# Kernel tuning notes

Hardware: AMD Instinct MI355X
Metric: run time of the kernel (lower is better)

## Reference

```python
import jax, jax.numpy as jnp
import numpy as np

C_IN = 1024
C_INTER = 512
EPS = 1e-5
STD = 0.01


def _conv1x1(x, w, b):
    # x: [B,C,H,W], w: [O,C] (1x1 conv kernel squeezed), b: [O]
    return jnp.einsum('bchw,oc->bohw', x, w) + b[None, :, None, None]


def setup_inputs() -> dict:
    key = jax.random.key(0)
    ks = jax.random.split(key, 12)
    def w(k, o, i):
        return jax.random.normal(k, (o, i), jnp.float32) * STD
    def b(k, o):
        return jax.random.normal(k, (o,), jnp.float32) * STD
    return {
        'x': jax.random.normal(ks[0], (8, C_IN, 64, 64), jnp.float32),
        'theta_w': w(ks[1], C_INTER, C_IN), 'theta_b': b(ks[2], C_INTER),
        'phi_w': w(ks[3], C_INTER, C_IN), 'phi_b': b(ks[4], C_INTER),
        'g_w': w(ks[5], C_INTER, C_IN), 'g_b': b(ks[6], C_INTER),
        'wz_w': w(ks[7], C_IN, C_INTER), 'wz_b': b(ks[8], C_IN),
        'bn_gamma': jax.random.normal(ks[9], (C_IN,), jnp.float32) * 0.1,
        'bn_beta': jax.random.normal(ks[10], (C_IN,), jnp.float32) * 0.1,
    }


def reference(x, theta_w, theta_b, phi_w, phi_b, g_w, g_b, wz_w, wz_b, bn_gamma, bn_beta):
    B, C, H, W = x.shape
    # theta on full-res input: [B, Ci, H*W]
    theta = _conv1x1(x, theta_w, theta_b).reshape(B, C_INTER, H * W)
    # 2x2 stride-2 max pool for phi/g path
    xp = jax.lax.reduce_window(x, -jnp.inf, jax.lax.max,
                               (1, 1, 2, 2), (1, 1, 2, 2), 'VALID')
    Hp, Wp = xp.shape[2], xp.shape[3]
    phi = _conv1x1(xp, phi_w, phi_b).reshape(B, C_INTER, Hp * Wp)
    g = _conv1x1(xp, g_w, g_b).reshape(B, C_INTER, Hp * Wp)
    # attention: [B, H*W, Hp*Wp], scaled softmax
    attn = jnp.einsum('bcn,bcm->bnm', theta, phi) * (C_INTER ** -0.5)
    attn = jax.nn.softmax(attn, axis=-1)
    # aggregate: [B, Ci, H*W]
    y = jnp.einsum('bcm,bnm->bcn', g, attn).reshape(B, C_INTER, H, W)
    z = _conv1x1(y, wz_w, wz_b)
    # BatchNorm2d (training-mode batch stats, biased var)
    mean = z.mean(axis=(0, 2, 3), keepdims=True)
    var = jnp.mean((z - mean) ** 2, axis=(0, 2, 3), keepdims=True)
    z = (z - mean) * jax.lax.rsqrt(var + EPS)
    z = z * bn_gamma[None, :, None, None] + bn_beta[None, :, None, None]
    return x + z
```

## Files before the change

### kernel.cpp

```cpp
#include <hip/hip_runtime.h>

typedef unsigned short u16;
typedef unsigned int u32;
typedef __attribute__((ext_vector_type(8))) short bf16x8;
typedef __attribute__((ext_vector_type(4))) float f32x4;

__device__ __forceinline__ u16 f2bf(float f) {
  u32 u = __builtin_bit_cast(u32, f);
  u = u + 0x7FFFu + ((u >> 16) & 1u);
  return (u16)(u >> 16);
}
__device__ __forceinline__ float bf2f(u16 s) {
  return __builtin_bit_cast(float, (u32)s << 16);
}

__device__ __forceinline__ void gload_lds16(const u16* g, u16* l) {
  __builtin_amdgcn_global_load_lds(
      (const __attribute__((address_space(1))) u32*)g,
      (__attribute__((address_space(3))) u32*)l, 16, 0, 0);
}

__global__ __launch_bounds__(256) void k_cvt4(
    const float* __restrict__ s0, const float* __restrict__ s1,
    const float* __restrict__ s2, const float* __restrict__ s3,
    u16* __restrict__ d0, u16* __restrict__ d1, u16* __restrict__ d2,
    u16* __restrict__ d3) {
  int gid = blockIdx.x * 256 + threadIdx.x;
  int which = gid >> 17;
  int loc = (gid & 131071) * 4;
  const float* s = which == 0 ? s0 : which == 1 ? s1 : which == 2 ? s2 : s3;
  u16* d = which == 0 ? d0 : which == 1 ? d1 : which == 2 ? d2 : d3;
  float4 v = *(const float4*)(s + loc);
  u32 lo = (u32)f2bf(v.x) | ((u32)f2bf(v.y) << 16);
  u32 hi = (u32)f2bf(v.z) | ((u32)f2bf(v.w) << 16);
  uint2 o; o.x = lo; o.y = hi;
  *(uint2*)(d + loc) = o;
}

__global__ __launch_bounds__(256) void k_transpose_pool(
    const float* __restrict__ x, u16* __restrict__ xT, u16* __restrict__ xpT) {
  __shared__ u16 lds[128 * 64];
  const int t = threadIdx.x;
  const int c0 = blockIdx.x * 64;
  const int by = blockIdx.y;
  const int b = blockIdx.z;

  {
    const int nf = (t & 31) * 4;
    const int swz = 8 * (t & 7);
    const float* xb =
        x + ((size_t)(b * 1024 + c0 + (t >> 5)) * 4096) + by * 128 + nf;
#pragma unroll
    for (int u = 0; u < 8; ++u) {
      const int c_l = (t >> 5) + 8 * u;
      float4 v = *(const float4*)(xb + (size_t)(8 * u) * 4096);
      const int col = c_l ^ swz;
      lds[(nf + 0) * 64 + col] = f2bf(v.x);
      lds[(nf + 1) * 64 + col] = f2bf(v.y);
      lds[(nf + 2) * 64 + col] = f2bf(v.z);
      lds[(nf + 3) * 64 + col] = f2bf(v.w);
    }
  }
  __syncthreads();
  {
#pragma unroll
    for (int v = 0; v < 4; ++v) {
      const int idx = t + 256 * v;
      const int n_l = idx >> 3;
      const int cb = (idx & 7) * 8;
      const int col = cb ^ (8 * ((n_l >> 2) & 7));
      bf16x8 d = *(const bf16x8*)&lds[n_l * 64 + col];
      *(bf16x8*)&xT[((size_t)b * 4096 + by * 128 + n_l) * 1024 + c0 + cb] = d;
    }
  }
  {
    const int m_w = t >> 3;
    const int cb = (t & 7) * 8;
    const int na = 2 * m_w, nb = na + 1, nc = na + 64, nd = na + 65;
    bf16x8 va = *(const bf16x8*)&lds[na * 64 + (cb ^ (8 * ((na >> 2) & 7)))];
    bf16x8 vb = *(const bf16x8*)&lds[nb * 64 + (cb ^ (8 * ((nb >> 2) & 7)))];
    bf16x8 vc = *(const bf16x8*)&lds[nc * 64 + (cb ^ (8 * ((nc >> 2) & 7)))];
    bf16x8 vd = *(const bf16x8*)&lds[nd * 64 + (cb ^ (8 * ((nd >> 2) & 7)))];
    bf16x8 o;
#pragma unroll
    for (int j = 0; j < 8; ++j) {
      float m = fmaxf(fmaxf(bf2f((u16)va[j]), bf2f((u16)vb[j])),
                      fmaxf(bf2f((u16)vc[j]), bf2f((u16)vd[j])));
      o[j] = (short)f2bf(m);
    }
    *(bf16x8*)&xpT[((size_t)b * 1024 + by * 32 + m_w) * 1024 + c0 + cb] = o;
  }
}

__global__ __launch_bounds__(256, 2) void gemm_dual(
    const u16* __restrict__ XPT, const u16* __restrict__ WP,
    const u16* __restrict__ WG, u16* __restrict__ PHI, u16* __restrict__ G,
    const float* __restrict__ phi_b, const float* __restrict__ g_b) {
  __shared__ u16 Alds[2][128 * 32];
  __shared__ u16 Blds[2][128 * 32];
  const int t = threadIdx.x;
  const int K = 1024;

  int id = blockIdx.x;
  const u16 *Ab, *Bb;
  u16* Cm;
  const float* bias;
  int N, bias_mode, bm, bn;
  if (id < 256) {
    bn = id & 3; bm = (id >> 2) & 7; const int b = id >> 5;
    Ab = XPT + (size_t)b * 1024 * 1024 + (size_t)bm * 128 * K;
    Bb = WP + (size_t)bn * 128 * K;
    Cm = PHI + (size_t)b * 1024 * 512;
    bias = phi_b; N = 512; bias_mode = 2;
  } else {
    id -= 256;
    bn = id & 7; bm = (id >> 3) & 3; const int b = id >> 5;
    Ab = WG + (size_t)bm * 128 * K;
    Bb = XPT + (size_t)b * 1024 * 1024 + (size_t)bn * 128 * K;
    Cm = G + (size_t)b * 512 * 1024;
    bias = g_b; N = 1024; bias_mode = 1;
  }

  const int lane = t & 63;
  const int w = t >> 6;
  const int wrow = w >> 1, wcol = w & 1;
  const int lr = lane & 15;
  const int kg = lane >> 4;

  f32x4 acc[4][4] = {};

  const int e0 = t * 8;
  const int r0 = e0 >> 5;
  const int k0i = e0 & 31;
  const int steps = K >> 5;

#define STAGE(buf, ks)                                                   \
  do {                                                                   \
    const int kb = (ks) * 32;                                            \
    gload_lds16(Ab + (size_t)r0 * K + kb + k0i, &Alds[buf][e0]);         \
    gload_lds16(Ab + (size_t)(r0 + 64) * K + kb + k0i,                   \
                &Alds[buf][e0 + 2048]);                                  \
    gload_lds16(Bb + (size_t)r0 * K + kb + k0i, &Blds[buf][e0]);         \
    gload_lds16(Bb + (size_t)(r0 + 64) * K + kb + k0i,                   \
                &Blds[buf][e0 + 2048]);                                  \
  } while (0)

  STAGE(0, 0);
  for (int ks = 0; ks < steps; ++ks) {
    const int cur = ks & 1;
    __syncthreads();
    if (ks + 1 < steps) STAGE(cur ^ 1, ks + 1);
    bf16x8 af[4], bfr[4];
#pragma unroll
    for (int i = 0; i < 4; ++i) {
      af[i] =
          *(const bf16x8*)&Alds[cur][(wrow * 64 + i * 16 + lr) * 32 + kg * 8];
      bfr[i] =
          *(const bf16x8*)&Blds[cur][(wcol * 64 + i * 16 + lr) * 32 + kg * 8];
    }
#pragma unroll
    for (int i = 0; i < 4; ++i)
#pragma unroll
      for (int j = 0; j < 4; ++j)
        acc[i][j] = __builtin_amdgcn_mfma_f32_16x16x32_bf16(af[i], bfr[j],
                                                            acc[i][j], 0, 0, 0);
  }
#undef STAGE

#pragma unroll
  for (int i = 0; i < 4; ++i) {
#pragma unroll
    for (int j = 0; j < 4; ++j) {
      int row0 = bm * 128 + wrow * 64 + i * 16 + kg * 4;
      int col = bn * 128 + wcol * 64 + j * 16 + lr;
      float bj = (bias_mode == 2) ? bias[col] : 0.f;
#pragma unroll
      for (int r = 0; r < 4; ++r) {
        float v = acc[i][j][r];
        v += (bias_mode == 1) ? bias[row0 + r] : bj;
        Cm[(size_t)(row0 + r) * N + col] = f2bf(v);
      }
    }
  }
}

template <int BIAS_MODE>
__global__ __launch_bounds__(512, 2) void gemm256(
    const u16* __restrict__ A, long aBS, const u16* __restrict__ Bm, long bBS,
    u16* __restrict__ Cm, long cBS, const float* __restrict__ bias, int N,
    int K, float scale) {
  __shared__ u16 ALDS[2][16384];
  __shared__ u16 BLDS[2][16384];
  const int t = threadIdx.x;
  u32 gx = gridDim.x, gy = gridDim.y;
  u32 nwg = gx * gy * gridDim.z;
  u32 wg = blockIdx.x + gx * (blockIdx.y + gy * blockIdx.z);
  u32 swz = (wg & 7) * (nwg >> 3) + (wg >> 3);
  const int bn = swz % gx;
  u32 tmp = swz / gx;
  const int bm = tmp % gy;
  const int b = tmp / gy;

  const u16* Agb = A + (size_t)b * aBS + (size_t)bm * 256 * K;
  const u16* Bgb = Bm + (size_t)b * bBS + (size_t)bn * 256 * K;

  const int lane = t & 63;
  const int wid = t >> 6;
  const int wr = wid >> 2;
  const int wc = wid & 3;
  const int lr = lane & 15;
  const int kg = (lane >> 4) & 3;
  const int T = K >> 6;

  f32x4 acc[8][4] = {};

#define STAGE_G(LDSARR, GB, h, ktn)                                          \
  if ((ktn) < T) {                                                           \
    {                                                                        \
      const int r = t >> 3;                                                  \
      gload_lds16(GB + (size_t)((h)*128 + r) * K + (size_t)(ktn)*64 +        \
                      (((t & 7) ^ (r & 7)) * 8),                             \
                  &LDSARR[(ktn) & 1][(h)*8192 + t * 8]);                     \
    }                                                                        \
    {                                                                        \
      const int idx = 512 + t;                                               \
      const int r = idx >> 3;                                                \
      gload_lds16(GB + (size_t)((h)*128 + r) * K + (size_t)(ktn)*64 +        \
                      (((t & 7) ^ (r & 7)) * 8),                             \
                  &LDSARR[(ktn) & 1][(h)*8192 + idx * 8]);                   \
    }                                                                        \
  }
#define STAGE_A(h, ktn) STAGE_G(ALDS, Agb, h, ktn)
#define STAGE_B(h, ktn) STAGE_G(BLDS, Bgb, h, ktn)

#define LDA4(mh, kk)                                                         \
  _Pragma("unroll") for (int m2 = 0; m2 < 4; ++m2) {                         \
    const int row = wr * 128 + ((mh)*4 + m2) * 16 + lr;                      \
    aF[m2] = *(const bf16x8*)&ALDS[cb][row * 64 +                            \
                                       ((((kk)*4 + kg) ^ (lr & 7)) * 8)];    \
  }
#define LDB4(kk)                                                             \
  _Pragma("unroll") for (int n = 0; n < 4; ++n) {                            \
    const int row = wc * 64 + n * 16 + lr;                                   \
    bF[n] = *(const bf16x8*)&BLDS[cb][row * 64 +                             \
                                      ((((kk)*4 + kg) ^ (lr & 7)) * 8)];     \
  }
#define MFMA16(M0)                                                           \
  __builtin_amdgcn_s_setprio(1);                                             \
  _Pragma("unroll") for (int n = 0; n < 4; ++n) {                            \
    acc[(M0) + 0][n] = __builtin_amdgcn_mfma_f32_16x16x32_bf16(              \
        aF[0], bF[n], acc[(M0) + 0][n], 0, 0, 0);                            \
    acc[(M0) + 1][n] = __builtin_amdgcn_mfma_f32_16x16x32_bf16(              \
        aF[1], bF[n], acc[(M0) + 1][n], 0, 0, 0);                            \
    acc[(M0) + 2][n] = __builtin_amdgcn_mfma_f32_16x16x32_bf16(              \
        aF[2], bF[n], acc[(M0) + 2][n], 0, 0, 0);                            \
    acc[(M0) + 3][n] = __builtin_amdgcn_mfma_f32_16x16x32_bf16(              \
        aF[3], bF[n], acc[(M0) + 3][n], 0, 0, 0);                            \
  }                                                                          \
  __builtin_amdgcn_s_setprio(0);
#define CFENCE asm volatile("" ::: "memory")

  STAGE_B(0, 0);
  STAGE_B(1, 0);
  STAGE_A(0, 0);
  STAGE_A(1, 0);
  STAGE_B(0, 1);

  for (int kt = 0; kt < T; ++kt) {
    const int cb = kt & 1;
    bf16x8 aF[4], bF[4];
    if (kt + 1 < T) {
      asm volatile("s_waitcnt vmcnt(2)" ::: "memory");
    } else {
      asm volatile("s_waitcnt vmcnt(0)" ::: "memory");
    }
    __builtin_amdgcn_s_barrier();
    STAGE_B(1, kt + 1);
    STAGE_A(0, kt + 1);
    STAGE_A(1, kt + 1);
    LDB4(0);
    LDA4(0, 0);
    MFMA16(0);
    CFENCE;
    __builtin_amdgcn_s_barrier();
    LDA4(1, 0);
    MFMA16(4);
    CFENCE;
    __builtin_amdgcn_s_barrier();
    LDB4(1);
    LDA4(0, 1);
    MFMA16(0);
    CFENCE;
    __builtin_amdgcn_s_barrier();
    STAGE_B(0, kt + 2);
    LDA4(1, 1);
    MFMA16(4);
    CFENCE;
    __builtin_amdgcn_s_barrier();
  }

  u16* Cb = Cm + (size_t)b * cBS;
#pragma unroll
  for (int m = 0; m < 8; ++m) {
    const int row0 = bm * 256 + wr * 128 + m * 16 + kg * 4;
#pragma unroll
    for (int n = 0; n < 4; ++n) {
      const int col = bn * 256 + wc * 64 + n * 16 + lr;
      float bj = (BIAS_MODE == 2) ? bias[col] : 0.f;
#pragma unroll
      for (int r = 0; r < 4; ++r) {
        float v = acc[m][n][r] * scale;
        if (BIAS_MODE == 1) v += bias[row0 + r];
        if (BIAS_MODE == 2) v += bj;
        Cb[(size_t)(row0 + r) * N + col] = f2bf(v);
      }
    }
  }
#undef STAGE_G
#undef STAGE_A
#undef STAGE_B
#undef LDA4
#undef LDB4
#undef MFMA16
#undef CFENCE
}

__global__ __launch_bounds__(256) void k_softmax(u16* __restrict__ S) {
  const int t = threadIdx.x;
  const int lane = t & 63;
  const size_t row = (size_t)blockIdx.x * 4 + (t >> 6);
  u16* p = S + row * 1024 + lane * 16;
  uint4 d0 = *(const uint4*)p;
  uint4 d1 = *(const uint4*)(p + 8);
  u32 u[8] = {d0.x, d0.y, d0.z, d0.w, d1.x, d1.y, d1.z, d1.w};
  float v[16];
#pragma unroll
  for (int i = 0; i < 8; ++i) {
    v[2 * i] = bf2f((u16)(u[i] & 0xffff));
    v[2 * i + 1] = bf2f((u16)(u[i] >> 16));
  }
  float m = v[0];
#pragma unroll
  for (int i = 1; i < 16; ++i) m = fmaxf(m, v[i]);
  for (int o = 32; o > 0; o >>= 1) m = fmaxf(m, __shfl_xor(m, o));
  const float LOG2E = 1.44269504088896f;
  float s = 0.f;
#pragma unroll
  for (int i = 0; i < 16; ++i) {
    v[i] = exp2f((v[i] - m) * LOG2E);
    s += v[i];
  }
  for (int o = 32; o > 0; o >>= 1) s += __shfl_xor(s, o);
  float inv = 1.0f / s;
#pragma unroll
  for (int i = 0; i < 8; ++i)
    u[i] = (u32)f2bf(v[2 * i] * inv) | ((u32)f2bf(v[2 * i + 1] * inv) << 16);
  uint4 o0; o0.x = u[0]; o0.y = u[1]; o0.z = u[2]; o0.w = u[3];
  uint4 o1; o1.x = u[4]; o1.y = u[5]; o1.z = u[6]; o1.w = u[7];
  *(uint4*)p = o0;
  *(uint4*)(p + 8) = o1;
}

__global__ __launch_bounds__(256) void k_stats(const u16* __restrict__ z,
                                               float2* __restrict__ stats) {
  const int o = blockIdx.x;
  const int t = threadIdx.x;
  float s = 0.f, q = 0.f;
  for (int b = 0; b < 8; ++b) {
    const u16* p = z + ((size_t)b * 1024 + o) * 4096;
    for (int i = t * 4; i < 4096; i += 1024) {
      uint2 d = *(const uint2*)(p + i);
      float a0 = bf2f((u16)(d.x & 0xffff)), a1 = bf2f((u16)(d.x >> 16));
      float a2 = bf2f((u16)(d.y & 0xffff)), a3 = bf2f((u16)(d.y >> 16));
      s += a0 + a1 + a2 + a3;
      q += a0 * a0 + a1 * a1 + a2 * a2 + a3 * a3;
    }
  }
  for (int o2 = 32; o2 > 0; o2 >>= 1) {
    s += __shfl_xor(s, o2);
    q += __shfl_xor(q, o2);
  }
  __shared__ float2 red[4];
  if ((t & 63) == 0) red[t >> 6] = make_float2(s, q);
  __syncthreads();
  if (t == 0) {
    float S_ = 0.f, Q_ = 0.f;
    for (int i = 0; i < 4; ++i) { S_ += red[i].x; Q_ += red[i].y; }
    stats[o] = make_float2(S_, Q_);
  }
}

__global__ __launch_bounds__(256) void k_apply(
    const float* __restrict__ x, const u16* __restrict__ z,
    const float2* __restrict__ stats, const float* __restrict__ gamma,
    const float* __restrict__ beta, float* __restrict__ out) {
  size_t i4 = (size_t)blockIdx.x * 256 + threadIdx.x;
  size_t e = i4 * 4;
  int c = (int)((e >> 12) & 1023);
  float2 st = stats[c];
  const float cnt = 1.0f / 32768.0f;
  float mean = st.x * cnt;
  float var = st.y * cnt - mean * mean;
  float g = rsqrtf(var + 1e-5f) * gamma[c];
  float sh = beta[c] - mean * g;
  float4 xv = *(const float4*)(x + e);
  uint2 zd = *(const uint2*)(z + e);
  float z0 = bf2f((u16)(zd.x & 0xffff)), z1 = bf2f((u16)(zd.x >> 16));
  float z2 = bf2f((u16)(zd.y & 0xffff)), z3 = bf2f((u16)(zd.y >> 16));
  float4 ov;
  ov.x = xv.x + z0 * g + sh;
  ov.y = xv.y + z1 * g + sh;
  ov.z = xv.z + z2 * g + sh;
  ov.w = xv.w + z3 * g + sh;
  *(float4*)(out + e) = ov;
}

extern "C" void kernel_launch(void* const* d_in, const int* in_sizes, int n_in,
                              void* d_out, int out_size, void* d_ws,
                              size_t ws_size, hipStream_t stream) {
  const float* x = (const float*)d_in[0];
  const float* theta_w = (const float*)d_in[1];
  const float* theta_b = (const float*)d_in[2];
  const float* phi_w = (const float*)d_in[3];
  const float* phi_b = (const float*)d_in[4];
  const float* g_w = (const float*)d_in[5];
  const float* g_b = (const float*)d_in[6];
  const float* wz_w = (const float*)d_in[7];
  const float* wz_b = (const float*)d_in[8];
  const float* gamma = (const float*)d_in[9];
  const float* beta = (const float*)d_in[10];
  float* out = (float*)d_out;

  char* w = (char*)d_ws;
  const size_t MiB = (size_t)1 << 20;
  u16* WT = (u16*)(w + 0 * MiB);
  u16* WP = (u16*)(w + 1 * MiB);
  u16* WG = (u16*)(w + 2 * MiB);
  u16* WZ = (u16*)(w + 3 * MiB);
  u16* XT = (u16*)(w + 4 * MiB);
  u16* XPT = (u16*)(w + 68 * MiB);
  u16* THETA = (u16*)(w + 84 * MiB);
  u16* PHI = (u16*)(w + 116 * MiB);
  u16* G = (u16*)(w + 124 * MiB);
  u16* S = XT;
  u16* YT = (u16*)(w + 132 * MiB);
  u16* Z = S;
  float2* stats = (float2*)(w + 164 * MiB);

  k_cvt4<<<2048, 256, 0, stream>>>(theta_w, phi_w, g_w, wz_w, WT, WP, WG, WZ);
  k_transpose_pool<<<dim3(16, 32, 8), 256, 0, stream>>>(x, XT, XPT);
  gemm256<2><<<dim3(2, 128, 1), 512, 0, stream>>>(
      XT, 0, WT, 0, THETA, 0, theta_b, 512, 1024, 1.0f);
  gemm_dual<<<512, 256, 0, stream>>>(XPT, WP, WG, PHI, G, phi_b, g_b);
  gemm256<0><<<dim3(4, 16, 8), 512, 0, stream>>>(
      THETA, (long)4096 * 512, PHI, (long)1024 * 512, S, (long)4096 * 1024,
      nullptr, 1024, 512, 0.04419417382415922f);
  k_softmax<<<8192, 256, 0, stream>>>(S);
  gemm256<0><<<dim3(2, 16, 8), 512, 0, stream>>>(
      S, (long)4096 * 1024, G, (long)512 * 1024, YT, (long)4096 * 512, nullptr,
      512, 1024, 1.0f);
  gemm256<1><<<dim3(16, 4, 8), 512, 0, stream>>>(
      WZ, 0, YT, (long)4096 * 512, Z, (long)1024 * 4096, wz_b, 4096, 512,
      1.0f);
  k_stats<<<1024, 256, 0, stream>>>(Z, stats);
  k_apply<<<32768, 256, 0, stream>>>(x, Z, stats, gamma, beta, out);

  (void)in_sizes; (void)n_in; (void)out_size; (void)ws_size;
}
```

Before: 549.1 us.

## Fuse softmax into attention GEMMs and BN stats into output GEMM

The separate softmax kernel is removed. The QK^T GEMM epilogue now writes exp of the scaled scores without max subtraction and atomically accumulates row sums, and the PV GEMM epilogue divides by those sums. The BatchNorm statistics kernel is replaced by per-row sum and sum-of-squares atomics in the Wz GEMM epilogue, with a small zeroing kernel added up front. The gemm_dual LDS layout also gains an XOR swizzle to reduce bank conflicts. Dropping the max subtraction risks overflow for larger logits, and the atomics add contention in exchange for removing two full passes over large intermediates.

```diff
diff --git a/kernel.cpp b/kernel.cpp
--- a/kernel.cpp
+++ b/kernel.cpp
@@ -18,6 +18,11 @@
   __builtin_amdgcn_global_load_lds(
       (const __attribute__((address_space(1))) u32*)g,
       (__attribute__((address_space(3))) u32*)l, 16, 0, 0);
+}
+
+__global__ __launch_bounds__(256) void k_zero_n(float* __restrict__ p) {
+  float4 z = {0.f, 0.f, 0.f, 0.f};
+  *(float4*)(p + (blockIdx.x * 256 + threadIdx.x) * 4) = z;
 }
 
 __global__ __launch_bounds__(256) void k_cvt4(
@@ -130,9 +135,11 @@
   f32x4 acc[4][4] = {};
 
   const int e0 = t * 8;
-  const int r0 = e0 >> 5;
-  const int k0i = e0 & 31;
+  const int r0 = t >> 2;
+  const int sl = (t & 3) ^ ((t >> 3) & 3);
+  const int k0i = sl * 8;
   const int steps = K >> 5;
+  const int rsw = (lr >> 1) & 3;
 
 #define STAGE(buf, ks)                                                   \
   do {                                                                   \
@@ -153,10 +160,10 @@
     bf16x8 af[4], bfr[4];
 #pragma unroll
     for (int i = 0; i < 4; ++i) {
-      af[i] =
-          *(const bf16x8*)&Alds[cur][(wrow * 64 + i * 16 + lr) * 32 + kg * 8];
-      bfr[i] =
-          *(const bf16x8*)&Blds[cur][(wcol * 64 + i * 16 + lr) * 32 + kg * 8];
+      af[i] = *(const bf16x8*)&Alds[cur][(wrow * 64 + i * 16 + lr) * 32 +
+                                         (kg ^ rsw) * 8];
+      bfr[i] = *(const bf16x8*)&Blds[cur][(wcol * 64 + i * 16 + lr) * 32 +
+                                          (kg ^ rsw) * 8];
     }
 #pragma unroll
     for (int i = 0; i < 4; ++i)
@@ -184,11 +191,11 @@
   }
 }
 
-template <int BIAS_MODE>
+template <int MODE>
 __global__ __launch_bounds__(512, 2) void gemm256(
     const u16* __restrict__ A, long aBS, const u16* __restrict__ Bm, long bBS,
     u16* __restrict__ Cm, long cBS, const float* __restrict__ bias, int N,
-    int K, float scale) {
+    int K, float scale, float* __restrict__ extra) {
   __shared__ u16 ALDS[2][16384];
   __shared__ u16 BLDS[2][16384];
   const int t = threadIdx.x;
@@ -300,19 +307,94 @@
   }
 
   u16* Cb = Cm + (size_t)b * cBS;
-#pragma unroll
-  for (int m = 0; m < 8; ++m) {
-    const int row0 = bm * 256 + wr * 128 + m * 16 + kg * 4;
-#pragma unroll
-    for (int n = 0; n < 4; ++n) {
-      const int col = bn * 256 + wc * 64 + n * 16 + lr;
-      float bj = (BIAS_MODE == 2) ? bias[col] : 0.f;
+  if constexpr (MODE == 2) {
+#pragma unroll
+    for (int m = 0; m < 8; ++m) {
+      const int row0 = bm * 256 + wr * 128 + m * 16 + kg * 4;
+#pragma unroll
+      for (int n = 0; n < 4; ++n) {
+        const int col = bn * 256 + wc * 64 + n * 16 + lr;
+        float bj = bias[col];
+#pragma unroll
+        for (int r = 0; r < 4; ++r)
+          Cb[(size_t)(row0 + r) * N + col] = f2bf(acc[m][n][r] + bj);
+      }
+    }
+  } else if constexpr (MODE == 3) {
+    const float c = scale * 1.44269504088896f;
+#pragma unroll
+    for (int m = 0; m < 8; ++m) {
+      const int row0 = bm * 256 + wr * 128 + m * 16 + kg * 4;
 #pragma unroll
       for (int r = 0; r < 4; ++r) {
-        float v = acc[m][n][r] * scale;
-        if (BIAS_MODE == 1) v += bias[row0 + r];
-        if (BIAS_MODE == 2) v += bj;
-        Cb[(size_t)(row0 + r) * N + col] = f2bf(v);
+        const int row = row0 + r;
+        float s = 0.f;
+#pragma unroll
+        for (int n = 0; n < 4; ++n) {
+          const int col = bn * 256 + wc * 64 + n * 16 + lr;
+          float v = exp2f(acc[m][n][r] * c);
+          Cb[(size_t)row * N + col] = f2bf(v);
+          s += v;
+        }
+        s += __shfl_xor(s, 1);
+        s += __shfl_xor(s, 2);
+        s += __shfl_xor(s, 4);
+        s += __shfl_xor(s, 8);
+        if (lr == 0) atomicAdd(&extra[(size_t)b * 4096 + row], s);
+      }
+    }
+  } else if constexpr (MODE == 4) {
+#pragma unroll
+    for (int m = 0; m < 8; ++m) {
+      const int row0 = bm * 256 + wr * 128 + m * 16 + kg * 4;
+#pragma unroll
+      for (int r = 0; r < 4; ++r) {
+        const int row = row0 + r;
+        const float inv = 1.0f / extra[(size_t)b * 4096 + row];
+#pragma unroll
+        for (int n = 0; n < 4; ++n) {
+          const int col = bn * 256 + wc * 64 + n * 16 + lr;
+          Cb[(size_t)row * N + col] = f2bf(acc[m][n][r] * inv);
+        }
+      }
+    }
+  } else {
+#pragma unroll
+    for (int m = 0; m < 8; ++m) {
+      const int row0 = bm * 256 + wr * 128 + m * 16 + kg * 4;
+#pragma unroll
+      for (int r = 0; r < 4; ++r) {
+        const int row = row0 + r;
+        const float bi = bias[row];
+#pragma unroll
+        for (int n = 0; n < 4; ++n) {
+          const int col = bn * 256 + wc * 64 + n * 16 + lr;
+          Cb[(size_t)row * N + col] = f2bf(acc[m][n][r] + bi);
+        }
+      }
+    }
+#pragma unroll
+    for (int m = 0; m < 8; ++m) {
+      const int row0 = bm * 256 + wr * 128 + m * 16 + kg * 4;
+#pragma unroll
+      for (int r = 0; r < 4; ++r) {
+        const int row = row0 + r;
+        const float bi = bias[row];
+        float s = 0.f, q = 0.f;
+#pragma unroll
+        for (int n = 0; n < 4; ++n) {
+          float v = acc[m][n][r] + bi;
+          s += v;
+          q += v * v;
+        }
+        s += __shfl_xor(s, 1); q += __shfl_xor(q, 1);
+        s += __shfl_xor(s, 2); q += __shfl_xor(q, 2);
+        s += __shfl_xor(s, 4); q += __shfl_xor(q, 4);
+        s += __shfl_xor(s, 8); q += __shfl_xor(q, 8);
+        if (lr == 0) {
+          atomicAdd(&extra[2 * row], s);
+          atomicAdd(&extra[2 * row + 1], q);
+        }
       }
     }
   }
@@ -323,71 +405,6 @@
 #undef LDB4
 #undef MFMA16
 #undef CFENCE
-}
-
-__global__ __launch_bounds__(256) void k_softmax(u16* __restrict__ S) {
-  const int t = threadIdx.x;
-  const int lane = t & 63;
-  const size_t row = (size_t)blockIdx.x * 4 + (t >> 6);
-  u16* p = S + row * 1024 + lane * 16;
-  uint4 d0 = *(const uint4*)p;
-  uint4 d1 = *(const uint4*)(p + 8);
-  u32 u[8] = {d0.x, d0.y, d0.z, d0.w, d1.x, d1.y, d1.z, d1.w};
-  float v[16];
-#pragma unroll
-  for (int i = 0; i < 8; ++i) {
-    v[2 * i] = bf2f((u16)(u[i] & 0xffff));
-    v[2 * i + 1] = bf2f((u16)(u[i] >> 16));
-  }
-  float m = v[0];
-#pragma unroll
-  for (int i = 1; i < 16; ++i) m = fmaxf(m, v[i]);
-  for (int o = 32; o > 0; o >>= 1) m = fmaxf(m, __shfl_xor(m, o));
-  const float LOG2E = 1.44269504088896f;
-  float s = 0.f;
-#pragma unroll
-  for (int i = 0; i < 16; ++i) {
-    v[i] = exp2f((v[i] - m) * LOG2E);
-    s += v[i];
-  }
-  for (int o = 32; o > 0; o >>= 1) s += __shfl_xor(s, o);
-  float inv = 1.0f / s;
-#pragma unroll
-  for (int i = 0; i < 8; ++i)
-    u[i] = (u32)f2bf(v[2 * i] * inv) | ((u32)f2bf(v[2 * i + 1] * inv) << 16);
-  uint4 o0; o0.x = u[0]; o0.y = u[1]; o0.z = u[2]; o0.w = u[3];
-  uint4 o1; o1.x = u[4]; o1.y = u[5]; o1.z = u[6]; o1.w = u[7];
-  *(uint4*)p = o0;
-  *(uint4*)(p + 8) = o1;
-}
-
-__global__ __launch_bounds__(256) void k_stats(const u16* __restrict__ z,
-                                               float2* __restrict__ stats) {
-  const int o = blockIdx.x;
-  const int t = threadIdx.x;
-  float s = 0.f, q = 0.f;
-  for (int b = 0; b < 8; ++b) {
-    const u16* p = z + ((size_t)b * 1024 + o) * 4096;
-    for (int i = t * 4; i < 4096; i += 1024) {
-      uint2 d = *(const uint2*)(p + i);
-      float a0 = bf2f((u16)(d.x & 0xffff)), a1 = bf2f((u16)(d.x >> 16));
-      float a2 = bf2f((u16)(d.y & 0xffff)), a3 = bf2f((u16)(d.y >> 16));
-      s += a0 + a1 + a2 + a3;
-      q += a0 * a0 + a1 * a1 + a2 * a2 + a3 * a3;
-    }
-  }
-  for (int o2 = 32; o2 > 0; o2 >>= 1) {
-    s += __shfl_xor(s, o2);
-    q += __shfl_xor(q, o2);
-  }
-  __shared__ float2 red[4];
-  if ((t & 63) == 0) red[t >> 6] = make_float2(s, q);
-  __syncthreads();
-  if (t == 0) {
-    float S_ = 0.f, Q_ = 0.f;
-    for (int i = 0; i < 4; ++i) { S_ += red[i].x; Q_ += red[i].y; }
-    stats[o] = make_float2(S_, Q_);
-  }
 }
 
 __global__ __launch_bounds__(256) void k_apply(
@@ -445,25 +462,26 @@
   u16* S = XT;
   u16* YT = (u16*)(w + 132 * MiB);
   u16* Z = S;
-  float2* stats = (float2*)(w + 164 * MiB);
-
+  float* stats = (float*)(w + 164 * MiB);
+  float* rowsum = stats + 2048;
+
+  k_zero_n<<<34, 256, 0, stream>>>(stats);
   k_cvt4<<<2048, 256, 0, stream>>>(theta_w, phi_w, g_w, wz_w, WT, WP, WG, WZ);
   k_transpose_pool<<<dim3(16, 32, 8), 256, 0, stream>>>(x, XT, XPT);
   gemm256<2><<<dim3(2, 128, 1), 512, 0, stream>>>(
-      XT, 0, WT, 0, THETA, 0, theta_b, 512, 1024, 1.0f);
+      XT, 0, WT, 0, THETA, 0, theta_b, 512, 1024, 1.0f, nullptr);
   gemm_dual<<<512, 256, 0, stream>>>(XPT, WP, WG, PHI, G, phi_b, g_b);
-  gemm256<0><<<dim3(4, 16, 8), 512, 0, stream>>>(
+  gemm256<3><<<dim3(4, 16, 8), 512, 0, stream>>>(
       THETA, (long)4096 * 512, PHI, (long)1024 * 512, S, (long)4096 * 1024,
-      nullptr, 1024, 512, 0.04419417382415922f);
-  k_softmax<<<8192, 256, 0, stream>>>(S);
-  gemm256<0><<<dim3(2, 16, 8), 512, 0, stream>>>(
+      nullptr, 1024, 512, 0.04419417382415922f, rowsum);
+  gemm256<4><<<dim3(2, 16, 8), 512, 0, stream>>>(
       S, (long)4096 * 1024, G, (long)512 * 1024, YT, (long)4096 * 512, nullptr,
-      512, 1024, 1.0f);
-  gemm256<1><<<dim3(16, 4, 8), 512, 0, stream>>>(
-      WZ, 0, YT, (long)4096 * 512, Z, (long)1024 * 4096, wz_b, 4096, 512,
-      1.0f);
-  k_stats<<<1024, 256, 0, stream>>>(Z, stats);
-  k_apply<<<32768, 256, 0, stream>>>(x, Z, stats, gamma, beta, out);
+      512, 1024, 1.0f, rowsum);
+  gemm256<5><<<dim3(16, 4, 8), 512, 0, stream>>>(
+      WZ, 0, YT, (long)4096 * 512, Z, (long)1024 * 4096, wz_b, 4096, 512, 1.0f,
+      stats);
+  k_apply<<<32768, 256, 0, stream>>>(x, Z, (const float2*)stats, gamma, beta,
+                                     out);
 
   (void)in_sizes; (void)n_in; (void)out_size; (void)ws_size;
 }
```

Measured after the change: 793.9 us. 44.6% more time.
